# Optimization experiments

Measured on AMD Instinct MI355X. Metric: run time of the kernel, lower is better.

The kernel has to match this reference:

```python
import jax, jax.numpy as jnp
import numpy as np

D_MODEL = 1024


def setup_inputs() -> dict:
    key = jax.random.key(0)
    k1, k2, k3 = jax.random.split(key, 3)
    x = jax.random.normal(k1, (8, 8192, D_MODEL), dtype=jnp.float32)
    mask = jax.random.randint(k2, (8, 8192), 0, 2).astype(jnp.bool_)  # True = padded
    query = jax.random.normal(k3, (1, 1, D_MODEL), dtype=jnp.float32)
    return {"x": x, "mask": mask, "query": query}


def reference(x, mask, query):
    # scores: (B, S) = sum_d query*x / sqrt(d_model)
    scale = jnp.sqrt(jnp.asarray(D_MODEL, x.dtype))
    scores = jnp.einsum("bsd,d->bs", x, query[0, 0]) / scale
    scores = jnp.where(mask, -jnp.inf, scores)
    weights = jax.nn.softmax(scores, axis=-1)  # (B, S)
    return jnp.einsum("bs,bsd->bd", weights, x)  # (B, d_model)
```

## Files before the change

### kernel.cpp

```cpp
#include <hip/hip_runtime.h>

#define D_MODEL 1024
#define NB 8
#define SEQ 8192
#define CHUNKS_PER_B 128
#define ROWS_PER_BLOCK 64
#define ROWS_PER_WAVE 16
#define THREADS 256
#define NEG_BIG (-1e30f)


__global__ __launch_bounds__(THREADS, 4)
void attn_partial(const float* __restrict__ x, const void* __restrict__ maskp,
                  const float* __restrict__ q, float* __restrict__ W)
{
    const int bid  = blockIdx.x;
    const int b    = bid >> 7;
    const int c    = bid & 127;
    const int tid  = threadIdx.x;
    const int lane = tid & 63;
    const int wv   = tid >> 6;

    __shared__ int   s_fmt;
    __shared__ float sm_m[4], sm_l[4];
    __shared__ float sm_acc[4][D_MODEL];

    if (tid == 0) s_fmt = 0;
    __syncthreads();
    if (((const unsigned int*)maskp)[tid] > 1u) s_fmt = 1;
    __syncthreads();
    const bool u8fmt = (s_fmt != 0);
    const unsigned char* m8  = (const unsigned char*)maskp;
    const int*           m32 = (const int*)maskp;

    const int    row0  = c * ROWS_PER_BLOCK + wv * ROWS_PER_WAVE;
    const size_t srow0 = (size_t)b * SEQ + row0;
    const float4* xw   = reinterpret_cast<const float4*>(x) + srow0 * (D_MODEL / 4);
    const float4* q4p  = reinterpret_cast<const float4*>(q);

    float4 q4[4], acc[4];
    #pragma unroll
    for (int k = 0; k < 4; ++k) {
        q4[k]  = q4p[k * 64 + lane];
        acc[k] = make_float4(0.f, 0.f, 0.f, 0.f);
    }
    float m_run = NEG_BIG, l_run = 0.f;

    for (int it = 0; it < ROWS_PER_WAVE / 2; ++it) {
        float4 xv[2][4];
        #pragma unroll
        for (int j = 0; j < 2; ++j)
            #pragma unroll
            for (int k = 0; k < 4; ++k)
                xv[j][k] = xw[(size_t)(it * 2 + j) * (D_MODEL / 4) + k * 64 + lane];

        float sc[2];
        #pragma unroll
        for (int j = 0; j < 2; ++j) {
            float d = xv[j][0].x * q4[0].x;
            d = fmaf(xv[j][0].y, q4[0].y, d);
            d = fmaf(xv[j][0].z, q4[0].z, d);
            d = fmaf(xv[j][0].w, q4[0].w, d);
            #pragma unroll
            for (int k = 1; k < 4; ++k) {
                d = fmaf(xv[j][k].x, q4[k].x, d);
                d = fmaf(xv[j][k].y, q4[k].y, d);
                d = fmaf(xv[j][k].z, q4[k].z, d);
                d = fmaf(xv[j][k].w, q4[k].w, d);
            }
            #pragma unroll
            for (int off = 32; off > 0; off >>= 1)
                d += __shfl_xor(d, off, 64);
            const int s = row0 + it * 2 + j;
            const int mv = u8fmt ? (int)m8[(size_t)b * SEQ + s] : m32[(size_t)b * SEQ + s];
            sc[j] = mv ? NEG_BIG : d * 0.03125f;
        }

        const float m_new = fmaxf(m_run, fmaxf(sc[0], sc[1]));
        const float resc  = __expf(m_run - m_new);
        l_run *= resc;
        const float w0 = __expf(sc[0] - m_new);
        const float w1 = __expf(sc[1] - m_new);
        l_run += w0 + w1;
        #pragma unroll
        for (int k = 0; k < 4; ++k) {
            acc[k].x = fmaf(w0, xv[0][k].x, fmaf(resc, 0.f, acc[k].x * resc));
            acc[k].x = fmaf(w1, xv[1][k].x, acc[k].x);
            acc[k].y = fmaf(w1, xv[1][k].y, fmaf(w0, xv[0][k].y, acc[k].y * resc));
            acc[k].z = fmaf(w1, xv[1][k].z, fmaf(w0, xv[0][k].z, acc[k].z * resc));
            acc[k].w = fmaf(w1, xv[1][k].w, fmaf(w0, xv[0][k].w, acc[k].w * resc));
        }
        m_run = m_new;
    }

    if (lane == 0) { sm_m[wv] = m_run; sm_l[wv] = l_run; }
    #pragma unroll
    for (int k = 0; k < 4; ++k)
        reinterpret_cast<float4*>(sm_acc[wv])[k * 64 + lane] = acc[k];
    __syncthreads();

    const float M = fmaxf(fmaxf(sm_m[0], sm_m[1]), fmaxf(sm_m[2], sm_m[3]));
    float f[4];
    #pragma unroll
    for (int w = 0; w < 4; ++w) f[w] = __expf(sm_m[w] - M);

    float4 o = make_float4(0.f, 0.f, 0.f, 0.f);
    #pragma unroll
    for (int w = 0; w < 4; ++w) {
        float4 a = reinterpret_cast<const float4*>(sm_acc[w])[wv * 64 + lane];
        o.x = fmaf(f[w], a.x, o.x);
        o.y = fmaf(f[w], a.y, o.y);
        o.z = fmaf(f[w], a.z, o.z);
        o.w = fmaf(f[w], a.w, o.w);
    }
    float* accOut = W + 2 * NB * CHUNKS_PER_B + (size_t)bid * D_MODEL;
    reinterpret_cast<float4*>(accOut)[wv * 64 + lane] = o;
    if (tid == 0) {
        W[bid] = M;
        W[NB * CHUNKS_PER_B + bid] = f[0] * sm_l[0] + f[1] * sm_l[1]
                                   + f[2] * sm_l[2] + f[3] * sm_l[3];
    }
}

__global__ __launch_bounds__(64)
void attn_combine(const float* __restrict__ W, float* __restrict__ out)
{
    const int b     = blockIdx.x >> 2;
    const int slice = blockIdx.x & 3;
    const int lane  = threadIdx.x;

    const float*  mArr = W + b * CHUNKS_PER_B;
    const float*  lArr = W + NB * CHUNKS_PER_B + b * CHUNKS_PER_B;
    const float4* accB = reinterpret_cast<const float4*>(
                             W + 2 * NB * CHUNKS_PER_B + (size_t)b * CHUNKS_PER_B * D_MODEL);

    __shared__ float s_f[CHUNKS_PER_B];

    const float m0 = mArr[lane], m1 = mArr[lane + 64];
    float M = fmaxf(m0, m1);
    #pragma unroll
    for (int off = 32; off > 0; off >>= 1) M = fmaxf(M, __shfl_xor(M, off, 64));

    const float f0 = __expf(m0 - M), f1 = __expf(m1 - M);
    s_f[lane] = f0; s_f[lane + 64] = f1;
    float L = fmaf(f0, lArr[lane], f1 * lArr[lane + 64]);
    #pragma unroll
    for (int off = 32; off > 0; off >>= 1) L += __shfl_xor(L, off, 64);
    __syncthreads();

    float4 o = make_float4(0.f, 0.f, 0.f, 0.f);
    #pragma unroll 8
    for (int k = 0; k < CHUNKS_PER_B; ++k) {
        const float  f = s_f[k];
        const float4 a = accB[(size_t)k * (D_MODEL / 4) + slice * 64 + lane];
        o.x = fmaf(f, a.x, o.x);
        o.y = fmaf(f, a.y, o.y);
        o.z = fmaf(f, a.z, o.z);
        o.w = fmaf(f, a.w, o.w);
    }
    const float inv = 1.f / L;
    reinterpret_cast<float4*>(out)[b * (D_MODEL / 4) + slice * 64 + lane] =
        make_float4(o.x * inv, o.y * inv, o.z * inv, o.w * inv);
}

extern "C" void kernel_launch(void* const* d_in, const int* in_sizes, int n_in,
                              void* d_out, int out_size, void* d_ws, size_t ws_size,
                              hipStream_t stream) {
    const float* x    = (const float*)d_in[0];
    const void*  mask = d_in[1];
    const float* q    = (const float*)d_in[2];
    float* out = (float*)d_out;
    float* W   = (float*)d_ws;

    attn_partial<<<NB * CHUNKS_PER_B, THREADS, 0, stream>>>(x, mask, q, W);
    attn_combine<<<NB * 4, 64, 0, stream>>>(W, out);
}
```

Before: 370.1 us.

## Fuse partial and combine kernels with atomic counter spin-wait

Merges the two launches into one grid, where 32 trailing combine blocks spin on an agent-scope atomic counter until all 1024 partial blocks have published their results. The combine phase now uses 256 threads and splits the chunk loop across waves, finishing with a shared-memory reduction. Mask values are preloaded once per wave and broadcast with a shuffle, and the format check uses a wave vote instead of shared memory plus two barriers. This removes the second kernel launch gap but adds a memset launch. It depends on the combine blocks not starving the partial blocks of scheduling slots, which could deadlock or add latency.

New measurement: 579.2 us. +56.5%, slower.

```diff
diff --git a/kernel.cpp b/kernel.cpp
--- a/kernel.cpp
+++ b/kernel.cpp
@@ -3,164 +3,196 @@
 #define D_MODEL 1024
 #define NB 8
 #define SEQ 8192
+#define PBLOCKS 1024
+#define CBLOCKS 32
 #define CHUNKS_PER_B 128
-#define ROWS_PER_BLOCK 64
-#define ROWS_PER_WAVE 16
 #define THREADS 256
 #define NEG_BIG (-1e30f)
 
 
 __global__ __launch_bounds__(THREADS, 4)
-void attn_partial(const float* __restrict__ x, const void* __restrict__ maskp,
-                  const float* __restrict__ q, float* __restrict__ W)
+void attn_fused(const float* __restrict__ x, const void* __restrict__ maskp,
+                const float* __restrict__ q, float* __restrict__ W,
+                unsigned int* __restrict__ counter, float* __restrict__ out)
 {
-    const int bid  = blockIdx.x;
-    const int b    = bid >> 7;
-    const int c    = bid & 127;
     const int tid  = threadIdx.x;
     const int lane = tid & 63;
     const int wv   = tid >> 6;
 
-    __shared__ int   s_fmt;
-    __shared__ float sm_m[4], sm_l[4];
-    __shared__ float sm_acc[4][D_MODEL];
-
-    if (tid == 0) s_fmt = 0;
-    __syncthreads();
-    if (((const unsigned int*)maskp)[tid] > 1u) s_fmt = 1;
-    __syncthreads();
-    const bool u8fmt = (s_fmt != 0);
-    const unsigned char* m8  = (const unsigned char*)maskp;
-    const int*           m32 = (const int*)maskp;
-
-    const int    row0  = c * ROWS_PER_BLOCK + wv * ROWS_PER_WAVE;
-    const size_t srow0 = (size_t)b * SEQ + row0;
-    const float4* xw   = reinterpret_cast<const float4*>(x) + srow0 * (D_MODEL / 4);
-    const float4* q4p  = reinterpret_cast<const float4*>(q);
-
-    float4 q4[4], acc[4];
-    #pragma unroll
-    for (int k = 0; k < 4; ++k) {
-        q4[k]  = q4p[k * 64 + lane];
-        acc[k] = make_float4(0.f, 0.f, 0.f, 0.f);
+    if (blockIdx.x < PBLOCKS) {
+        const int bid = blockIdx.x;
+        const int b   = bid >> 7;
+        const int c   = bid & 127;
+
+        __shared__ float sm_m[4], sm_l[4];
+        __shared__ float sm_acc[4][D_MODEL];
+
+        const bool u8fmt = __any(((const unsigned int*)maskp)[lane] > 1u);
+        const unsigned char* m8  = (const unsigned char*)maskp;
+        const int*           m32 = (const int*)maskp;
+
+        const int     row0 = c * 64 + wv * 16;
+        const float4* xw   = (const float4*)x + ((size_t)b * SEQ + row0) * (D_MODEL / 4);
+        const float4* q4p  = (const float4*)q;
+
+        int mraw = 0;
+        if (lane < 16) {
+            const size_t mi = (size_t)b * SEQ + row0 + lane;
+            mraw = u8fmt ? (int)m8[mi] : m32[mi];
+        }
+
+        float4 q4[4], acc[4];
+        #pragma unroll
+        for (int k = 0; k < 4; ++k) {
+            q4[k]  = q4p[k * 64 + lane];
+            acc[k] = make_float4(0.f, 0.f, 0.f, 0.f);
+        }
+        float m_run = NEG_BIG, l_run = 0.f;
+
+        #pragma unroll 2
+        for (int it = 0; it < 8; ++it) {
+            float4 xv[2][4];
+            #pragma unroll
+            for (int j = 0; j < 2; ++j)
+                #pragma unroll
+                for (int k = 0; k < 4; ++k)
+                    xv[j][k] = xw[(size_t)(it * 2 + j) * (D_MODEL / 4) + k * 64 + lane];
+
+            float sc[2];
+            #pragma unroll
+            for (int j = 0; j < 2; ++j) {
+                float d = xv[j][0].x * q4[0].x;
+                d = fmaf(xv[j][0].y, q4[0].y, d);
+                d = fmaf(xv[j][0].z, q4[0].z, d);
+                d = fmaf(xv[j][0].w, q4[0].w, d);
+                #pragma unroll
+                for (int k = 1; k < 4; ++k) {
+                    d = fmaf(xv[j][k].x, q4[k].x, d);
+                    d = fmaf(xv[j][k].y, q4[k].y, d);
+                    d = fmaf(xv[j][k].z, q4[k].z, d);
+                    d = fmaf(xv[j][k].w, q4[k].w, d);
+                }
+                #pragma unroll
+                for (int off = 32; off > 0; off >>= 1)
+                    d += __shfl_xor(d, off, 64);
+                const int mv = __shfl(mraw, it * 2 + j, 64);
+                sc[j] = mv ? NEG_BIG : d * 0.03125f;
+            }
+
+            const float m_new = fmaxf(m_run, fmaxf(sc[0], sc[1]));
+            const float resc  = __expf(m_run - m_new);
+            const float w0    = __expf(sc[0] - m_new);
+            const float w1    = __expf(sc[1] - m_new);
+            l_run = fmaf(l_run, resc, w0 + w1);
+            #pragma unroll
+            for (int k = 0; k < 4; ++k) {
+                acc[k].x = fmaf(w1, xv[1][k].x, fmaf(w0, xv[0][k].x, acc[k].x * resc));
+                acc[k].y = fmaf(w1, xv[1][k].y, fmaf(w0, xv[0][k].y, acc[k].y * resc));
+                acc[k].z = fmaf(w1, xv[1][k].z, fmaf(w0, xv[0][k].z, acc[k].z * resc));
+                acc[k].w = fmaf(w1, xv[1][k].w, fmaf(w0, xv[0][k].w, acc[k].w * resc));
+            }
+            m_run = m_new;
+        }
+
+        if (lane == 0) { sm_m[wv] = m_run; sm_l[wv] = l_run; }
+        #pragma unroll
+        for (int k = 0; k < 4; ++k)
+            reinterpret_cast<float4*>(sm_acc[wv])[k * 64 + lane] = acc[k];
+        __syncthreads();
+
+        const float M = fmaxf(fmaxf(sm_m[0], sm_m[1]), fmaxf(sm_m[2], sm_m[3]));
+        float f[4];
+        #pragma unroll
+        for (int w = 0; w < 4; ++w) f[w] = __expf(sm_m[w] - M);
+
+        float4 o = make_float4(0.f, 0.f, 0.f, 0.f);
+        #pragma unroll
+        for (int w = 0; w < 4; ++w) {
+            float4 a = reinterpret_cast<const float4*>(sm_acc[w])[wv * 64 + lane];
+            o.x = fmaf(f[w], a.x, o.x);
+            o.y = fmaf(f[w], a.y, o.y);
+            o.z = fmaf(f[w], a.z, o.z);
+            o.w = fmaf(f[w], a.w, o.w);
+        }
+        float* accOut = W + 2 * PBLOCKS + (size_t)bid * D_MODEL;
+        reinterpret_cast<float4*>(accOut)[wv * 64 + lane] = o;
+        if (tid == 0) {
+            W[bid] = M;
+            W[PBLOCKS + bid] = f[0] * sm_l[0] + f[1] * sm_l[1]
+                             + f[2] * sm_l[2] + f[3] * sm_l[3];
+        }
+
+        __threadfence();
+        __syncthreads();
+        if (tid == 0)
+            __hip_atomic_fetch_add(counter, 1u, __ATOMIC_RELEASE, __HIP_MEMORY_SCOPE_AGENT);
+    } else {
+        const int cb = blockIdx.x - PBLOCKS;
+        const int b  = cb >> 2;
+        const int cs = cb & 3;
+
+        __shared__ float  s_f[CHUNKS_PER_B];
+        __shared__ float  s_red[4];
+        __shared__ float4 s_o[4][64];
+
+        if (tid == 0) {
+            while (__hip_atomic_load(counter, __ATOMIC_ACQUIRE,
+                                     __HIP_MEMORY_SCOPE_AGENT) < (unsigned)PBLOCKS)
+                __builtin_amdgcn_s_sleep(8);
+        }
+        __syncthreads();
+
+        const float*  mArr = W + b * CHUNKS_PER_B;
+        const float*  lArr = W + PBLOCKS + b * CHUNKS_PER_B;
+        const float4* accB = (const float4*)(W + 2 * PBLOCKS)
+                           + (size_t)b * CHUNKS_PER_B * (D_MODEL / 4);
+
+        const float mv = (tid < CHUNKS_PER_B) ? mArr[tid] : NEG_BIG;
+        float mr = mv;
+        #pragma unroll
+        for (int off = 32; off > 0; off >>= 1) mr = fmaxf(mr, __shfl_xor(mr, off, 64));
+        if (lane == 0) s_red[wv] = mr;
+        __syncthreads();
+        const float M = fmaxf(fmaxf(s_red[0], s_red[1]), fmaxf(s_red[2], s_red[3]));
+        __syncthreads();
+
+        float Lp = 0.f;
+        if (tid < CHUNKS_PER_B) {
+            const float fk = __expf(mv - M);
+            s_f[tid] = fk;
+            Lp = fk * lArr[tid];
+        }
+        #pragma unroll
+        for (int off = 32; off > 0; off >>= 1) Lp += __shfl_xor(Lp, off, 64);
+        if (lane == 0) s_red[wv] = Lp;
+        __syncthreads();
+        const float L = s_red[0] + s_red[1] + s_red[2] + s_red[3];
+
+        const int p = cs * 64 + lane;
+        float4 o = make_float4(0.f, 0.f, 0.f, 0.f);
+        #pragma unroll 4
+        for (int kk = 0; kk < 32; ++kk) {
+            const int    k = wv * 32 + kk;
+            const float  fk = s_f[k];
+            const float4 a  = accB[(size_t)k * (D_MODEL / 4) + p];
+            o.x = fmaf(fk, a.x, o.x);
+            o.y = fmaf(fk, a.y, o.y);
+            o.z = fmaf(fk, a.z, o.z);
+            o.w = fmaf(fk, a.w, o.w);
+        }
+        s_o[wv][lane] = o;
+        __syncthreads();
+        if (wv == 0) {
+            float4 r;
+            r.x = s_o[0][lane].x + s_o[1][lane].x + s_o[2][lane].x + s_o[3][lane].x;
+            r.y = s_o[0][lane].y + s_o[1][lane].y + s_o[2][lane].y + s_o[3][lane].y;
+            r.z = s_o[0][lane].z + s_o[1][lane].z + s_o[2][lane].z + s_o[3][lane].z;
+            r.w = s_o[0][lane].w + s_o[1][lane].w + s_o[2][lane].w + s_o[3][lane].w;
+            const float inv = 1.f / L;
+            reinterpret_cast<float4*>(out)[b * (D_MODEL / 4) + p] =
+                make_float4(r.x * inv, r.y * inv, r.z * inv, r.w * inv);
+        }
     }
-    float m_run = NEG_BIG, l_run = 0.f;
-
-    for (int it = 0; it < ROWS_PER_WAVE / 2; ++it) {
-        float4 xv[2][4];
-        #pragma unroll
-        for (int j = 0; j < 2; ++j)
-            #pragma unroll
-            for (int k = 0; k < 4; ++k)
-                xv[j][k] = xw[(size_t)(it * 2 + j) * (D_MODEL / 4) + k * 64 + lane];
-
-        float sc[2];
-        #pragma unroll
-        for (int j = 0; j < 2; ++j) {
-            float d = xv[j][0].x * q4[0].x;
-            d = fmaf(xv[j][0].y, q4[0].y, d);
-            d = fmaf(xv[j][0].z, q4[0].z, d);
-            d = fmaf(xv[j][0].w, q4[0].w, d);
-            #pragma unroll
-            for (int k = 1; k < 4; ++k) {
-                d = fmaf(xv[j][k].x, q4[k].x, d);
-                d = fmaf(xv[j][k].y, q4[k].y, d);
-                d = fmaf(xv[j][k].z, q4[k].z, d);
-                d = fmaf(xv[j][k].w, q4[k].w, d);
-            }
-            #pragma unroll
-            for (int off = 32; off > 0; off >>= 1)
-                d += __shfl_xor(d, off, 64);
-            const int s = row0 + it * 2 + j;
-            const int mv = u8fmt ? (int)m8[(size_t)b * SEQ + s] : m32[(size_t)b * SEQ + s];
-            sc[j] = mv ? NEG_BIG : d * 0.03125f;
-        }
-
-        const float m_new = fmaxf(m_run, fmaxf(sc[0], sc[1]));
-        const float resc  = __expf(m_run - m_new);
-        l_run *= resc;
-        const float w0 = __expf(sc[0] - m_new);
-        const float w1 = __expf(sc[1] - m_new);
-        l_run += w0 + w1;
-        #pragma unroll
-        for (int k = 0; k < 4; ++k) {
-            acc[k].x = fmaf(w0, xv[0][k].x, fmaf(resc, 0.f, acc[k].x * resc));
-            acc[k].x = fmaf(w1, xv[1][k].x, acc[k].x);
-            acc[k].y = fmaf(w1, xv[1][k].y, fmaf(w0, xv[0][k].y, acc[k].y * resc));
-            acc[k].z = fmaf(w1, xv[1][k].z, fmaf(w0, xv[0][k].z, acc[k].z * resc));
-            acc[k].w = fmaf(w1, xv[1][k].w, fmaf(w0, xv[0][k].w, acc[k].w * resc));
-        }
-        m_run = m_new;
-    }
-
-    if (lane == 0) { sm_m[wv] = m_run; sm_l[wv] = l_run; }
-    #pragma unroll
-    for (int k = 0; k < 4; ++k)
-        reinterpret_cast<float4*>(sm_acc[wv])[k * 64 + lane] = acc[k];
-    __syncthreads();
-
-    const float M = fmaxf(fmaxf(sm_m[0], sm_m[1]), fmaxf(sm_m[2], sm_m[3]));
-    float f[4];
-    #pragma unroll
-    for (int w = 0; w < 4; ++w) f[w] = __expf(sm_m[w] - M);
-
-    float4 o = make_float4(0.f, 0.f, 0.f, 0.f);
-    #pragma unroll
-    for (int w = 0; w < 4; ++w) {
-        float4 a = reinterpret_cast<const float4*>(sm_acc[w])[wv * 64 + lane];
-        o.x = fmaf(f[w], a.x, o.x);
-        o.y = fmaf(f[w], a.y, o.y);
-        o.z = fmaf(f[w], a.z, o.z);
-        o.w = fmaf(f[w], a.w, o.w);
-    }
-    float* accOut = W + 2 * NB * CHUNKS_PER_B + (size_t)bid * D_MODEL;
-    reinterpret_cast<float4*>(accOut)[wv * 64 + lane] = o;
-    if (tid == 0) {
-        W[bid] = M;
-        W[NB * CHUNKS_PER_B + bid] = f[0] * sm_l[0] + f[1] * sm_l[1]
-                                   + f[2] * sm_l[2] + f[3] * sm_l[3];
-    }
-}
-
-__global__ __launch_bounds__(64)
-void attn_combine(const float* __restrict__ W, float* __restrict__ out)
-{
-    const int b     = blockIdx.x >> 2;
-    const int slice = blockIdx.x & 3;
-    const int lane  = threadIdx.x;
-
-    const float*  mArr = W + b * CHUNKS_PER_B;
-    const float*  lArr = W + NB * CHUNKS_PER_B + b * CHUNKS_PER_B;
-    const float4* accB = reinterpret_cast<const float4*>(
-                             W + 2 * NB * CHUNKS_PER_B + (size_t)b * CHUNKS_PER_B * D_MODEL);
-
-    __shared__ float s_f[CHUNKS_PER_B];
-
-    const float m0 = mArr[lane], m1 = mArr[lane + 64];
-    float M = fmaxf(m0, m1);
-    #pragma unroll
-    for (int off = 32; off > 0; off >>= 1) M = fmaxf(M, __shfl_xor(M, off, 64));
-
-    const float f0 = __expf(m0 - M), f1 = __expf(m1 - M);
-    s_f[lane] = f0; s_f[lane + 64] = f1;
-    float L = fmaf(f0, lArr[lane], f1 * lArr[lane + 64]);
-    #pragma unroll
-    for (int off = 32; off > 0; off >>= 1) L += __shfl_xor(L, off, 64);
-    __syncthreads();
-
-    float4 o = make_float4(0.f, 0.f, 0.f, 0.f);
-    #pragma unroll 8
-    for (int k = 0; k < CHUNKS_PER_B; ++k) {
-        const float  f = s_f[k];
-        const float4 a = accB[(size_t)k * (D_MODEL / 4) + slice * 64 + lane];
-        o.x = fmaf(f, a.x, o.x);
-        o.y = fmaf(f, a.y, o.y);
-        o.z = fmaf(f, a.z, o.z);
-        o.w = fmaf(f, a.w, o.w);
-    }
-    const float inv = 1.f / L;
-    reinterpret_cast<float4*>(out)[b * (D_MODEL / 4) + slice * 64 + lane] =
-        make_float4(o.x * inv, o.y * inv, o.z * inv, o.w * inv);
 }
 
 extern "C" void kernel_launch(void* const* d_in, const int* in_sizes, int n_in,
@@ -169,9 +201,10 @@
     const float* x    = (const float*)d_in[0];
     const void*  mask = d_in[1];
     const float* q    = (const float*)d_in[2];
-    float* out = (float*)d_out;
-    float* W   = (float*)d_ws;
-
-    attn_partial<<<NB * CHUNKS_PER_B, THREADS, 0, stream>>>(x, mask, q, W);
-    attn_combine<<<NB * 4, 64, 0, stream>>>(W, out);
+    float*        out = (float*)d_out;
+    unsigned int* ctr = (unsigned int*)d_ws;
+    float*        W   = (float*)((char*)d_ws + 64);
+
+    hipMemsetAsync(d_ws, 0, 64, stream);
+    attn_fused<<<PBLOCKS + CBLOCKS, THREADS, 0, stream>>>(x, mask, q, W, ctr, out);
 }
```

## Process four rows per iteration, batch shuffles, and preload mask per wave

Applied to the files above, without the earlier changes.

The per-wave loop now loads four x rows per iteration instead of two, so more memory requests are in flight per wave. The four dot-product reductions are interleaved across the shuffle steps to shorten the dependent shuffle chain. The mask is loaded once per wave into lanes and broadcast with a shuffle rather than read per row, and the block-wide mask-format detection barriers become a wave-level __any. More registers per thread may reduce occupancy under the launch bound.

Result: no change. 367.7 us (median of 2 runs) (-0.7%).

```diff
diff --git a/kernel.cpp b/kernel.cpp
--- a/kernel.cpp
+++ b/kernel.cpp
@@ -4,8 +4,6 @@
 #define NB 8
 #define SEQ 8192
 #define CHUNKS_PER_B 128
-#define ROWS_PER_BLOCK 64
-#define ROWS_PER_WAVE 16
 #define THREADS 256
 #define NEG_BIG (-1e30f)
 
@@ -21,22 +19,22 @@
     const int lane = tid & 63;
     const int wv   = tid >> 6;
 
-    __shared__ int   s_fmt;
     __shared__ float sm_m[4], sm_l[4];
     __shared__ float sm_acc[4][D_MODEL];
 
-    if (tid == 0) s_fmt = 0;
-    __syncthreads();
-    if (((const unsigned int*)maskp)[tid] > 1u) s_fmt = 1;
-    __syncthreads();
-    const bool u8fmt = (s_fmt != 0);
+    const bool u8fmt = __any(((const unsigned int*)maskp)[lane] > 1u);
     const unsigned char* m8  = (const unsigned char*)maskp;
     const int*           m32 = (const int*)maskp;
 
-    const int    row0  = c * ROWS_PER_BLOCK + wv * ROWS_PER_WAVE;
-    const size_t srow0 = (size_t)b * SEQ + row0;
-    const float4* xw   = reinterpret_cast<const float4*>(x) + srow0 * (D_MODEL / 4);
-    const float4* q4p  = reinterpret_cast<const float4*>(q);
+    const int     row0 = c * 64 + wv * 16;
+    const float4* xw   = (const float4*)x + ((size_t)b * SEQ + row0) * (D_MODEL / 4);
+    const float4* q4p  = (const float4*)q;
+
+    int mraw = 0;
+    if (lane < 16) {
+        const size_t mi = (size_t)b * SEQ + row0 + lane;
+        mraw = u8fmt ? (int)m8[mi] : m32[mi];
+    }
 
     float4 q4[4], acc[4];
     #pragma unroll
@@ -46,17 +44,17 @@
     }
     float m_run = NEG_BIG, l_run = 0.f;
 
-    for (int it = 0; it < ROWS_PER_WAVE / 2; ++it) {
-        float4 xv[2][4];
+    for (int it = 0; it < 4; ++it) {
+        float4 xv[4][4];
         #pragma unroll
-        for (int j = 0; j < 2; ++j)
+        for (int j = 0; j < 4; ++j)
             #pragma unroll
             for (int k = 0; k < 4; ++k)
-                xv[j][k] = xw[(size_t)(it * 2 + j) * (D_MODEL / 4) + k * 64 + lane];
+                xv[j][k] = xw[(size_t)(it * 4 + j) * (D_MODEL / 4) + k * 64 + lane];
 
-        float sc[2];
+        float sc[4];
         #pragma unroll
-        for (int j = 0; j < 2; ++j) {
+        for (int j = 0; j < 4; ++j) {
             float d = xv[j][0].x * q4[0].x;
             d = fmaf(xv[j][0].y, q4[0].y, d);
             d = fmaf(xv[j][0].z, q4[0].z, d);
@@ -68,27 +66,37 @@
                 d = fmaf(xv[j][k].z, q4[k].z, d);
                 d = fmaf(xv[j][k].w, q4[k].w, d);
             }
+            sc[j] = d;
+        }
+        #pragma unroll
+        for (int off = 32; off > 0; off >>= 1) {
             #pragma unroll
-            for (int off = 32; off > 0; off >>= 1)
-                d += __shfl_xor(d, off, 64);
-            const int s = row0 + it * 2 + j;
-            const int mv = u8fmt ? (int)m8[(size_t)b * SEQ + s] : m32[(size_t)b * SEQ + s];
-            sc[j] = mv ? NEG_BIG : d * 0.03125f;
+            for (int j = 0; j < 4; ++j)
+                sc[j] += __shfl_xor(sc[j], off, 64);
+        }
+        #pragma unroll
+        for (int j = 0; j < 4; ++j) {
+            const int mv = __shfl(mraw, it * 4 + j, 64);
+            sc[j] = mv ? NEG_BIG : sc[j] * 0.03125f;
         }
 
-        const float m_new = fmaxf(m_run, fmaxf(sc[0], sc[1]));
-        const float resc  = __expf(m_run - m_new);
-        l_run *= resc;
-        const float w0 = __expf(sc[0] - m_new);
-        const float w1 = __expf(sc[1] - m_new);
-        l_run += w0 + w1;
+        const float m_new = fmaxf(m_run,
+                                  fmaxf(fmaxf(sc[0], sc[1]), fmaxf(sc[2], sc[3])));
+        const float resc = __expf(m_run - m_new);
+        float w[4];
+        #pragma unroll
+        for (int j = 0; j < 4; ++j) w[j] = __expf(sc[j] - m_new);
+        l_run = fmaf(l_run, resc, (w[0] + w[1]) + (w[2] + w[3]));
         #pragma unroll
         for (int k = 0; k < 4; ++k) {
-            acc[k].x = fmaf(w0, xv[0][k].x, fmaf(resc, 0.f, acc[k].x * resc));
-            acc[k].x = fmaf(w1, xv[1][k].x, acc[k].x);
-            acc[k].y = fmaf(w1, xv[1][k].y, fmaf(w0, xv[0][k].y, acc[k].y * resc));
-            acc[k].z = fmaf(w1, xv[1][k].z, fmaf(w0, xv[0][k].z, acc[k].z * resc));
-            acc[k].w = fmaf(w1, xv[1][k].w, fmaf(w0, xv[0][k].w, acc[k].w * resc));
+            acc[k].x = fmaf(w[3], xv[3][k].x, fmaf(w[2], xv[2][k].x,
+                       fmaf(w[1], xv[1][k].x, fmaf(w[0], xv[0][k].x, acc[k].x * resc))));
+            acc[k].y = fmaf(w[3], xv[3][k].y, fmaf(w[2], xv[2][k].y,
+                       fmaf(w[1], xv[1][k].y, fmaf(w[0], xv[0][k].y, acc[k].y * resc))));
+            acc[k].z = fmaf(w[3], xv[3][k].z, fmaf(w[2], xv[2][k].z,
+                       fmaf(w[1], xv[1][k].z, fmaf(w[0], xv[0][k].z, acc[k].z * resc))));
+            acc[k].w = fmaf(w[3], xv[3][k].w, fmaf(w[2], xv[2][k].w,
+                       fmaf(w[1], xv[1][k].w, fmaf(w[0], xv[0][k].w, acc[k].w * resc))));
         }
         m_run = m_new;
     }
```
